# Performance work log

Measured on AMD Instinct MI355X. Metric: run time of the kernel, lower is better.

The kernel has to match this reference:

```python
import jax, jax.numpy as jnp
import numpy as np

COLUMN_BLOCK = 64  # bits_in_a_channel(256) // 4


def _pack(bits_blk):
    # bits_blk: uint16 (b, H, n_blocks, D, column_block) -- cache layout
    first8 = (bits_blk >> 8).astype(jnp.uint8)                      # sign+exp+2 mantissa bits
    mid = ((bits_blk >> 4) & 0xF).astype(jnp.uint8)                 # next 4 mantissa bits
    last = (bits_blk & 0xF).astype(jnp.uint8)                       # last 4 mantissa bits
    mid4 = (mid[..., 0::2] << 4) | mid[..., 1::2]                   # two columns per byte
    last4 = (last[..., 0::2] << 4) | last[..., 1::2]
    return first8, mid4, last4


def _unpack(first8, mid4, last4):
    shp = first8.shape
    mid = jnp.stack([mid4 >> 4, mid4 & 0xF], axis=-1).reshape(shp)
    last = jnp.stack([last4 >> 4, last4 & 0xF], axis=-1).reshape(shp)
    rbits = (first8.astype(jnp.uint16) << 8) | (mid.astype(jnp.uint16) << 4) | last.astype(jnp.uint16)
    return jax.lax.bitcast_convert_type(rbits, jnp.float16)


def setup_inputs() -> dict:
    key = jax.random.key(0)
    k1, k2 = jax.random.split(key)
    bsz, max_seq_len, n_kv, d_head = 8, 8192, 8, 128
    new_k = jax.random.normal(k1, (bsz, max_seq_len, n_kv, d_head), dtype=jnp.float16)
    q = jax.random.normal(k2, (bsz, 1, n_kv, d_head), dtype=jnp.float16)
    return {"new_k": new_k, "q": q, "start_pos": 8191, "seqlen": 1}


def reference(new_k, q, start_pos, seqlen):
    # Prefill save(new_k, 0, S) followed by decoding_compute(q, start_pos, seqlen)
    b, S, H, D = new_k.shape
    nb = S // COLUMN_BLOCK
    total = start_pos + seqlen  # number of valid cached positions

    # ---- save path: bit-plane packing into the blocked cache layout ----
    bits = jax.lax.bitcast_convert_type(new_k, jnp.uint16)          # (b,S,H,D)
    # per-column max exponent tracking (mirrors k_cache_exp_column_max)
    exp = ((bits >> 10) & 31).astype(jnp.uint8)
    k_exp_col_max = jnp.max(exp, axis=1, keepdims=True)             # (b,1,H,D)
    # blocked layout: (b, H, n_blocks, D, column_block)
    bits_blk = bits.reshape(b, nb, COLUMN_BLOCK, H, D).transpose(0, 3, 1, 4, 2)
    first8, mid4, last4 = _pack(bits_blk)

    # ---- compute path (reference=True: exact reconstruction from planes) ----
    q_exp = ((jax.lax.bitcast_convert_type(q, jnp.uint16) >> 10) & 31).astype(jnp.uint8)
    _ = q_exp + k_exp_col_max  # exponent bookkeeping (drives precision in fast path)
    k_rec = _unpack(first8, mid4, last4)                            # (b,H,nb,D,cb) fp16

    s = jnp.einsum('bqhd,bhndc->bhqnc',
                   q.astype(jnp.float32), k_rec.astype(jnp.float32))
    s = (s.reshape(b, H, q.shape[1], S) * np.float32(1.0 / np.sqrt(D))).astype(jnp.float16)
    pos = jnp.arange(S)
    s = jnp.where(pos[None, None, None, :] < total, s, jnp.float16(-jnp.inf))
    return s
```

## Files before the change

kernel.cpp:

```cpp
#include <hip/hip_runtime.h>
#include <hip/hip_fp16.h>


#define S_LEN 8192
#define NH    8
#define DH    128
#define HPT   2
#define BLK   256

__global__ __launch_bounds__(BLK) void qk_decode_kernel(
    const float* __restrict__ K,
    const float* __restrict__ Q,
    const int* __restrict__ sp,
    const int* __restrict__ sl,
    float* __restrict__ out)
{
    const int b  = blockIdx.y;
    const int h0 = blockIdx.z * HPT;
    const int s  = blockIdx.x * BLK + threadIdx.x;

    __shared__ float qs[HPT * DH];
    for (int i = threadIdx.x; i < HPT * DH; i += BLK)
        qs[i] = Q[((size_t)b * NH + h0) * DH + i];
    __syncthreads();

    const float4* krow = (const float4*)(K + (((size_t)b * S_LEN + s) * NH + h0) * DH);

    float acc[HPT];
#pragma unroll
    for (int h = 0; h < HPT; ++h) {
        const float4* p  = krow + h * (DH / 4);
        const float*  qp = &qs[h * DH];
        float a0 = 0.f, a1 = 0.f, a2 = 0.f, a3 = 0.f;
#pragma unroll
        for (int c = 0; c < DH / 4; c += 4) {
            float4 v0 = p[c], v1 = p[c + 1], v2 = p[c + 2], v3 = p[c + 3];
            a0 += v0.x * qp[4*c+ 0] + v0.y * qp[4*c+ 1] + v0.z * qp[4*c+ 2] + v0.w * qp[4*c+ 3];
            a1 += v1.x * qp[4*c+ 4] + v1.y * qp[4*c+ 5] + v1.z * qp[4*c+ 6] + v1.w * qp[4*c+ 7];
            a2 += v2.x * qp[4*c+ 8] + v2.y * qp[4*c+ 9] + v2.z * qp[4*c+10] + v2.w * qp[4*c+11];
            a3 += v3.x * qp[4*c+12] + v3.y * qp[4*c+13] + v3.z * qp[4*c+14] + v3.w * qp[4*c+15];
        }
        acc[h] = (a0 + a1) + (a2 + a3);
    }

    const int total = sp[0] + sl[0];
    const float scale = 0.08838834764831845f;

#pragma unroll
    for (int h = 0; h < HPT; ++h) {
        float o;
        if (s < total) {
            o = __half2float(__float2half(acc[h] * scale));
        } else {
            o = -INFINITY;
        }
        out[((size_t)b * NH + h0 + h) * S_LEN + s] = o;
    }
}

extern "C" void kernel_launch(void* const* d_in, const int* in_sizes, int n_in,
                              void* d_out, int out_size, void* d_ws, size_t ws_size,
                              hipStream_t stream) {
    const float* K  = (const float*)d_in[0];
    const float* Q  = (const float*)d_in[1];
    const int*   sp = (const int*)d_in[2];
    const int*   sl = (const int*)d_in[3];
    float* out = (float*)d_out;

    dim3 grid(S_LEN / BLK, 8 , NH / HPT);
    dim3 block(BLK);
    qk_decode_kernel<<<grid, block, 0, stream>>>(K, Q, sp, sl, out);
}
```

Baseline: 387.5 us.

## Coalesce K loads with per-wavefront row reads and shuffle reductions

Each wavefront now processes 16 sequence positions, with its 64 lanes reading consecutive float4 chunks of a full position row across all heads, instead of each thread striding through its own row. Per-head dot products are reduced with xor shuffles across 32 lanes, and Q is held in registers rather than shared memory. This targets uncoalesced global loads in a bandwidth-bound kernel, at the cost of shuffle work and scattered single-lane output stores.

```diff
diff --git a/kernel.cpp b/kernel.cpp
--- a/kernel.cpp
+++ b/kernel.cpp
@@ -5,69 +5,74 @@
 #define S_LEN 8192
 #define NH    8
 #define DH    128
-#define HPT   2
+#define ROW4  (NH * DH / 4)
+#define PPW   16
 #define BLK   256
 
 __global__ __launch_bounds__(BLK) void qk_decode_kernel(
-    const float* __restrict__ K,
-    const float* __restrict__ Q,
+    const float4* __restrict__ K4,
+    const float4* __restrict__ Q4,
     const int* __restrict__ sp,
     const int* __restrict__ sl,
     float* __restrict__ out)
 {
-    const int b  = blockIdx.y;
-    const int h0 = blockIdx.z * HPT;
-    const int s  = blockIdx.x * BLK + threadIdx.x;
+    const int lane = threadIdx.x & 63;
+    const int wid  = threadIdx.x >> 6;
+    const int b    = blockIdx.y;
+    const int s0   = (blockIdx.x * 4 + wid) * PPW;
 
-    __shared__ float qs[HPT * DH];
-    for (int i = threadIdx.x; i < HPT * DH; i += BLK)
-        qs[i] = Q[((size_t)b * NH + h0) * DH + i];
-    __syncthreads();
+    float4 qr[4];
+#pragma unroll
+    for (int g = 0; g < 4; ++g)
+        qr[g] = Q4[b * ROW4 + g * 64 + lane];
 
-    const float4* krow = (const float4*)(K + (((size_t)b * S_LEN + s) * NH + h0) * DH);
+    const int   total   = sp[0] + sl[0];
+    const float scale   = 0.08838834764831845f;
+    const int   halfsel = lane >> 5;
+    const bool  writer  = (lane & 31) == 0;
 
-    float acc[HPT];
+    const float4* kbase = K4 + (size_t)b * S_LEN * ROW4;
+
+#pragma unroll 2
+    for (int ps = 0; ps < PPW; ++ps) {
+        const int s = s0 + ps;
+        const float4* row = kbase + (size_t)s * ROW4;
+
+        float part[4];
 #pragma unroll
-    for (int h = 0; h < HPT; ++h) {
-        const float4* p  = krow + h * (DH / 4);
-        const float*  qp = &qs[h * DH];
-        float a0 = 0.f, a1 = 0.f, a2 = 0.f, a3 = 0.f;
-#pragma unroll
-        for (int c = 0; c < DH / 4; c += 4) {
-            float4 v0 = p[c], v1 = p[c + 1], v2 = p[c + 2], v3 = p[c + 3];
-            a0 += v0.x * qp[4*c+ 0] + v0.y * qp[4*c+ 1] + v0.z * qp[4*c+ 2] + v0.w * qp[4*c+ 3];
-            a1 += v1.x * qp[4*c+ 4] + v1.y * qp[4*c+ 5] + v1.z * qp[4*c+ 6] + v1.w * qp[4*c+ 7];
-            a2 += v2.x * qp[4*c+ 8] + v2.y * qp[4*c+ 9] + v2.z * qp[4*c+10] + v2.w * qp[4*c+11];
-            a3 += v3.x * qp[4*c+12] + v3.y * qp[4*c+13] + v3.z * qp[4*c+14] + v3.w * qp[4*c+15];
+        for (int g = 0; g < 4; ++g) {
+            float4 v = row[g * 64 + lane];
+            part[g] = v.x * qr[g].x + v.y * qr[g].y + v.z * qr[g].z + v.w * qr[g].w;
         }
-        acc[h] = (a0 + a1) + (a2 + a3);
-    }
-
-    const int total = sp[0] + sl[0];
-    const float scale = 0.08838834764831845f;
 
 #pragma unroll
-    for (int h = 0; h < HPT; ++h) {
-        float o;
-        if (s < total) {
-            o = __half2float(__float2half(acc[h] * scale));
-        } else {
-            o = -INFINITY;
+        for (int g = 0; g < 4; ++g) {
+            float p = part[g];
+            p += __shfl_xor(p, 1);
+            p += __shfl_xor(p, 2);
+            p += __shfl_xor(p, 4);
+            p += __shfl_xor(p, 8);
+            p += __shfl_xor(p, 16);
+            if (writer) {
+                float o = (s < total)
+                        ? __half2float(__float2half(p * scale))
+                        : -INFINITY;
+                out[((size_t)b * NH + 2 * g + halfsel) * S_LEN + s] = o;
+            }
         }
-        out[((size_t)b * NH + h0 + h) * S_LEN + s] = o;
     }
 }
 
 extern "C" void kernel_launch(void* const* d_in, const int* in_sizes, int n_in,
                               void* d_out, int out_size, void* d_ws, size_t ws_size,
                               hipStream_t stream) {
-    const float* K  = (const float*)d_in[0];
-    const float* Q  = (const float*)d_in[1];
-    const int*   sp = (const int*)d_in[2];
-    const int*   sl = (const int*)d_in[3];
+    const float4* K4 = (const float4*)d_in[0];
+    const float4* Q4 = (const float4*)d_in[1];
+    const int*    sp = (const int*)d_in[2];
+    const int*    sl = (const int*)d_in[3];
     float* out = (float*)d_out;
 
-    dim3 grid(S_LEN / BLK, 8 , NH / HPT);
+    dim3 grid(S_LEN / (PPW * 4), 8 );
     dim3 block(BLK);
-    qk_decode_kernel<<<grid, block, 0, stream>>>(K, Q, sp, sl, out);
+    qk_decode_kernel<<<grid, block, 0, stream>>>(K4, Q4, sp, sl, out);
 }
```

After: 364.7 us. 5.9% less time.
